# Optimization experiments

Hardware: AMD Instinct MI355X
Metric: run time of the kernel (lower is better)

## Reference

```python
import jax, jax.numpy as jnp
import numpy as np

N, E, D, H = 100000, 1000000, 64, 64  # nodes, edges, input_dim, output_dim
EPS = 1e-5


def _lin(k, fi, fo):
    return jax.random.normal(k, (fi, fo), jnp.float32) / np.sqrt(fi)


def setup_inputs() -> dict:
    key = jax.random.key(0)
    ks = jax.random.split(key, 8)
    x = jax.random.normal(ks[0], (N, D), jnp.float32)
    e = jax.random.uniform(ks[1], (E,), jnp.float32)
    edge_index = jax.random.randint(ks[2], (2, E), 0, N, dtype=jnp.int32)
    return {
        "x": x,
        "e": e,
        "edge_index": edge_index,
        "W1": _lin(ks[3], 2 * D, H), "b1": jnp.zeros((H,), jnp.float32),
        "g1": jnp.ones((H,), jnp.float32), "be1": jnp.zeros((H,), jnp.float32),
        "W2": _lin(ks[4], H, H), "b2": jnp.zeros((H,), jnp.float32),
        "g2": jnp.ones((H,), jnp.float32), "be2": jnp.zeros((H,), jnp.float32),
        "W3": _lin(ks[5], H, H), "b3": jnp.zeros((H,), jnp.float32),
    }


def _layer_norm(h, g, b):
    mu = jnp.mean(h, axis=-1, keepdims=True)
    var = jnp.mean(jnp.square(h - mu), axis=-1, keepdims=True)
    return (h - mu) * jax.lax.rsqrt(var + EPS) * g + b


def reference(x, e, edge_index, W1, b1, g1, be1, W2, b2, g2, be2, W3, b3):
    start, end = edge_index[0], edge_index[1]
    we = e[:, None]  # [E,1]
    # edge-weighted gather-multiply-scatter_add, both directions
    mi = jax.ops.segment_sum(we * x[start], end, num_segments=N) \
       + jax.ops.segment_sum(we * x[end], start, num_segments=N)  # [N,D]
    h = jnp.concatenate([mi, x], axis=1)  # [N,2D]
    h = jnp.tanh(_layer_norm(h @ W1 + b1, g1, be1))
    h = jnp.tanh(_layer_norm(h @ W2 + b2, g2, be2))
    return h @ W3 + b3  # [N,H]
```

## Files before the change

kernel.cpp:

```cpp
#include <hip/hip_runtime.h>

typedef unsigned int u32;
typedef int   v4i __attribute__((ext_vector_type(4)));
typedef float v4f __attribute__((ext_vector_type(4)));

#define NMAX 100000
#define EMAX 1000000
#define CAP 64
#define NSHMAX 12500

__device__ __align__(16) float g_mi[NMAX * 64];
__device__ int g_deg[8 * NSHMAX];
__device__ __align__(16) u32 g_adj[(size_t)8 * NSHMAX * CAP];

__global__ __launch_bounds__(256) void fill_sharded(
    const int* __restrict__ src, const int* __restrict__ dst,
    const float* __restrict__ ew, int E, int NSH, int nchunk)
{
    int group = blockIdx.x & 7;
    int chunk = blockIdx.x >> 3;
    int stride = nchunk * 256 * 4;
    for (int e0 = (chunk * 256 + threadIdx.x) * 4; e0 < E; e0 += stride) {
        if (e0 + 3 < E) {
            v4i s4 = __builtin_nontemporal_load((const v4i*)&src[e0]);
            v4i t4 = __builtin_nontemporal_load((const v4i*)&dst[e0]);
            v4f w4 = __builtin_nontemporal_load((const v4f*)&ew[e0]);
            #pragma unroll
            for (int j = 0; j < 4; j++) {
                int s = s4[j], t = t4[j];
                float w = w4[j];
                int w15 = (int)(w * 32768.f + 0.5f);
                if (w15 > 32767) w15 = 32767;
                if ((s & 7) == group) {
                    int idx = group * NSH + (s >> 3);
                    int p = atomicAdd(&g_deg[idx], 1);
                    if (p < CAP) g_adj[(size_t)idx * CAP + p] = ((u32)t << 15) | (u32)w15;
                }
                if ((t & 7) == group) {
                    int idx = group * NSH + (t >> 3);
                    int q = atomicAdd(&g_deg[idx], 1);
                    if (q < CAP) g_adj[(size_t)idx * CAP + q] = ((u32)s << 15) | (u32)w15;
                }
            }
        } else {
            for (int e = e0; e < E; e++) {
                int s = src[e], t = dst[e];
                float w = ew[e];
                int w15 = (int)(w * 32768.f + 0.5f);
                if (w15 > 32767) w15 = 32767;
                if ((s & 7) == group) {
                    int idx = group * NSH + (s >> 3);
                    int p = atomicAdd(&g_deg[idx], 1);
                    if (p < CAP) g_adj[(size_t)idx * CAP + p] = ((u32)t << 15) | (u32)w15;
                }
                if ((t & 7) == group) {
                    int idx = group * NSH + (t >> 3);
                    int q = atomicAdd(&g_deg[idx], 1);
                    if (q < CAP) g_adj[(size_t)idx * CAP + q] = ((u32)s << 15) | (u32)w15;
                }
            }
        }
    }
}

__global__ __launch_bounds__(256) void gather(const float* __restrict__ x,
                                              int N, int NSH) {
    int wid = (blockIdx.x * 256 + threadIdx.x) >> 6;
    int lane = threadIdx.x & 63;
    if (wid >= N) return;
    int idx = (wid & 7) * NSH + (wid >> 3);
    int cnt = g_deg[idx];
    if (lane == 0) g_deg[idx] = 0;
    if (cnt > CAP) cnt = CAP;
    const u32* row = g_adj + (size_t)idx * CAP;
    float acc = 0.f;

    for (int b = 0; b < cnt; b += 64) {
        int m = cnt - b;
        if (m > 64) m = 64;
        u32 ent = (lane < m) ? row[b + lane] : 0u;
        int nbr = (int)(ent >> 15);
        float wv = (float)(ent & 0x7FFFu) * (1.f / 32768.f);

        int j = 0;
        for (; j + 8 <= m; j += 8) {
            int   nn[8];
            float ww[8];
            #pragma unroll
            for (int u = 0; u < 8; u++) { nn[u] = __shfl(nbr, j + u); ww[u] = __shfl(wv, j + u); }
            float vv[8];
            #pragma unroll
            for (int u = 0; u < 8; u++) vv[u] = x[(size_t)nn[u] * 64 + lane];
            #pragma unroll
            for (int u = 0; u < 8; u++) acc = fmaf(ww[u], vv[u], acc);
        }
        for (; j + 4 <= m; j += 4) {
            int n0 = __shfl(nbr, j + 0);
            int n1 = __shfl(nbr, j + 1);
            int n2 = __shfl(nbr, j + 2);
            int n3 = __shfl(nbr, j + 3);
            float w0 = __shfl(wv, j + 0);
            float w1 = __shfl(wv, j + 1);
            float w2 = __shfl(wv, j + 2);
            float w3 = __shfl(wv, j + 3);
            float v0 = x[(size_t)n0 * 64 + lane];
            float v1 = x[(size_t)n1 * 64 + lane];
            float v2 = x[(size_t)n2 * 64 + lane];
            float v3 = x[(size_t)n3 * 64 + lane];
            acc = fmaf(w0, v0, acc);
            acc = fmaf(w1, v1, acc);
            acc = fmaf(w2, v2, acc);
            acc = fmaf(w3, v3, acc);
        }
        for (; j < m; j++) {
            int nb = __shfl(nbr, j);
            float w = __shfl(wv, j);
            acc = fmaf(w, x[(size_t)nb * 64 + lane], acc);
        }
    }
    g_mi[(size_t)wid * 64 + lane] = acc;
}

#define HS 68
#define SWF(f) ((((f) >> 2) & 7) << 2)

#define GEMM_PASS(WP) do {                                              \
    _Pragma("unroll 2")                                                 \
    for (int k = 0; k < 64; k++) {                                      \
        float a = ht[k * HS + (lane ^ SWF(k))];                         \
        const float* wp = (WP) + k * 64 + c0;                           \
        _Pragma("unroll")                                               \
        for (int c = 0; c < 16; c++) acc[c] = fmaf(a, wp[c], acc[c]);   \
    } } while (0)

__global__ __launch_bounds__(256, 8) void mlp(
    const float* __restrict__ x,
    const float* __restrict__ W1, const float* __restrict__ B1,
    const float* __restrict__ G1, const float* __restrict__ E1,
    const float* __restrict__ W2, const float* __restrict__ B2,
    const float* __restrict__ G2, const float* __restrict__ E2,
    const float* __restrict__ W3, const float* __restrict__ B3,
    float* __restrict__ out, int N)
{
    __shared__ float ht[64 * HS];
    __shared__ float lnb[4 * 64];

    int tid  = threadIdx.x;
    int lane = tid & 63;
    int c0   = __builtin_amdgcn_readfirstlane(tid >> 6) * 16;
    int n0 = blockIdx.x * 64;
    int nodes = N - n0; if (nodes > 64) nodes = 64;

    if (tid < 64) {
        lnb[tid]       = G1[tid];
        lnb[64 + tid]  = E1[tid];
        lnb[128 + tid] = G2[tid];
        lnb[192 + tid] = E2[tid];
    }

    float acc[16];
    #pragma unroll
    for (int c = 0; c < 16; c++) acc[c] = B1[c0 + c];

    #pragma unroll
    for (int it = 0; it < 4; it++) {
        int idx = tid + it * 256;
        int nd = idx >> 4, f4 = (idx & 15) * 4;
        v4f v = {0.f, 0.f, 0.f, 0.f};
        if (nd < nodes) v = *(const v4f*)&g_mi[(size_t)(n0 + nd) * 64 + f4];
        ht[(f4 + 0) * HS + (nd ^ SWF(f4 + 0))] = v[0];
        ht[(f4 + 1) * HS + (nd ^ SWF(f4 + 1))] = v[1];
        ht[(f4 + 2) * HS + (nd ^ SWF(f4 + 2))] = v[2];
        ht[(f4 + 3) * HS + (nd ^ SWF(f4 + 3))] = v[3];
    }
    __syncthreads();
    GEMM_PASS(W1);
    __syncthreads();

    #pragma unroll
    for (int it = 0; it < 4; it++) {
        int idx = tid + it * 256;
        int nd = idx >> 4, f4 = (idx & 15) * 4;
        v4f v = {0.f, 0.f, 0.f, 0.f};
        if (nd < nodes) v = *(const v4f*)&x[(size_t)(n0 + nd) * 64 + f4];
        ht[(f4 + 0) * HS + (nd ^ SWF(f4 + 0))] = v[0];
        ht[(f4 + 1) * HS + (nd ^ SWF(f4 + 1))] = v[1];
        ht[(f4 + 2) * HS + (nd ^ SWF(f4 + 2))] = v[2];
        ht[(f4 + 3) * HS + (nd ^ SWF(f4 + 3))] = v[3];
    }
    __syncthreads();
    GEMM_PASS(W1 + 64 * 64);
    __syncthreads();

    #pragma unroll
    for (int c = 0; c < 16; c++)
        ht[(c0 + c) * HS + (lane ^ SWF(c0 + c))] = acc[c];
    __syncthreads();

    if (tid < 64) {
        float mu = 0.f;
        for (int j = 0; j < 64; j++) mu += ht[j * HS + (tid ^ SWF(j))];
        mu *= (1.f / 64.f);
        float var = 0.f;
        for (int j = 0; j < 64; j++) { float d = ht[j * HS + (tid ^ SWF(j))] - mu; var += d * d; }
        var *= (1.f / 64.f);
        float rs = rsqrtf(var + 1e-5f);
        for (int j = 0; j < 64; j++) {
            float v = (ht[j * HS + (tid ^ SWF(j))] - mu) * rs * lnb[j] + lnb[64 + j];
            float ex = __expf(2.f * v);
            ht[j * HS + (tid ^ SWF(j))] = 1.f - 2.f / (ex + 1.f);
        }
    }
    __syncthreads();

    #pragma unroll
    for (int c = 0; c < 16; c++) acc[c] = B2[c0 + c];
    GEMM_PASS(W2);
    __syncthreads();
    #pragma unroll
    for (int c = 0; c < 16; c++)
        ht[(c0 + c) * HS + (lane ^ SWF(c0 + c))] = acc[c];
    __syncthreads();

    if (tid < 64) {
        float mu = 0.f;
        for (int j = 0; j < 64; j++) mu += ht[j * HS + (tid ^ SWF(j))];
        mu *= (1.f / 64.f);
        float var = 0.f;
        for (int j = 0; j < 64; j++) { float d = ht[j * HS + (tid ^ SWF(j))] - mu; var += d * d; }
        var *= (1.f / 64.f);
        float rs = rsqrtf(var + 1e-5f);
        for (int j = 0; j < 64; j++) {
            float v = (ht[j * HS + (tid ^ SWF(j))] - mu) * rs * lnb[128 + j] + lnb[192 + j];
            float ex = __expf(2.f * v);
            ht[j * HS + (tid ^ SWF(j))] = 1.f - 2.f / (ex + 1.f);
        }
    }
    __syncthreads();

    #pragma unroll
    for (int c = 0; c < 16; c++) acc[c] = B3[c0 + c];
    GEMM_PASS(W3);
    __syncthreads();
    #pragma unroll
    for (int c = 0; c < 16; c++)
        ht[(c0 + c) * HS + (lane ^ SWF(c0 + c))] = acc[c];
    __syncthreads();

    #pragma unroll
    for (int it = 0; it < 4; it++) {
        int idx = tid + it * 256;
        int nd = idx >> 4, f4 = (idx & 15) * 4;
        if (nd < nodes) {
            v4f v = { ht[(f4 + 0) * HS + (nd ^ SWF(f4 + 0))],
                      ht[(f4 + 1) * HS + (nd ^ SWF(f4 + 1))],
                      ht[(f4 + 2) * HS + (nd ^ SWF(f4 + 2))],
                      ht[(f4 + 3) * HS + (nd ^ SWF(f4 + 3))] };
            *(v4f*)&out[(size_t)(n0 + nd) * 64 + f4] = v;
        }
    }
}

extern "C" void kernel_launch(void* const* d_in, const int* in_sizes, int n_in,
                              void* d_out, int out_size, void* d_ws, size_t ws_size,
                              hipStream_t stream) {
    const float* x  = (const float*)d_in[0];
    const float* e  = (const float*)d_in[1];
    const int* ei   = (const int*)d_in[2];
    const float* W1 = (const float*)d_in[3];
    const float* b1 = (const float*)d_in[4];
    const float* g1 = (const float*)d_in[5];
    const float* be1= (const float*)d_in[6];
    const float* W2 = (const float*)d_in[7];
    const float* b2 = (const float*)d_in[8];
    const float* g2 = (const float*)d_in[9];
    const float* be2= (const float*)d_in[10];
    const float* W3 = (const float*)d_in[11];
    const float* b3 = (const float*)d_in[12];

    int N = in_sizes[0] / 64;
    int E = in_sizes[1];
    int NSH = (N + 7) / 8;

    int nchunk = 256;
    fill_sharded<<<8 * nchunk, 256, 0, stream>>>(ei, ei + E, e, E, NSH, nchunk);

    gather<<<(N * 64 + 255) / 256, 256, 0, stream>>>(x, N, NSH);

    mlp<<<(N + 63) / 64, 256, 0, stream>>>(
        x, W1, b1, g1, be1, W2, b2, g2, be2, W3, b3, (float*)d_out, N);
}
```

Before: 333.2 us.

## Gather four nodes per wavefront with 16-lane groups and float4 loads

The gather kernel now assigns four nodes to each 64-lane wavefront, with 16 lanes per node, and each lane loads a float4 of the neighbour's feature row instead of a single float. The goal is more memory-level parallelism per wave, wider loads, and fewer wavefronts for low-degree nodes. Every group in a wave iterates up to the wave's maximum degree in steps of 16. Invalid slots read the node's own row with zero weight, which adds redundant loads when degrees differ.

```diff
diff --git a/kernel.cpp b/kernel.cpp
--- a/kernel.cpp
+++ b/kernel.cpp
@@ -63,62 +63,46 @@
     }
 }
 
-__global__ __launch_bounds__(256) void gather(const float* __restrict__ x,
-                                              int N, int NSH) {
-    int wid = (blockIdx.x * 256 + threadIdx.x) >> 6;
+__global__ __launch_bounds__(256) void gather4(const float* __restrict__ x,
+                                               int N, int NSH) {
+    int wid  = (blockIdx.x * 256 + threadIdx.x) >> 6;
     int lane = threadIdx.x & 63;
-    if (wid >= N) return;
-    int idx = (wid & 7) * NSH + (wid >> 3);
-    int cnt = g_deg[idx];
-    if (lane == 0) g_deg[idx] = 0;
+    int sub  = lane >> 4;
+    int q    = lane & 15;
+    int node = wid * 4 + sub;
+    if (wid * 4 >= N) return;
+    bool nvalid = node < N;
+    int nodec = nvalid ? node : N - 1;
+    int idx = (nodec & 7) * NSH + (nodec >> 3);
+    int cnt = nvalid ? g_deg[idx] : 0;
+    if (nvalid && q == 0) g_deg[idx] = 0;
     if (cnt > CAP) cnt = CAP;
     const u32* row = g_adj + (size_t)idx * CAP;
-    float acc = 0.f;
-
-    for (int b = 0; b < cnt; b += 64) {
-        int m = cnt - b;
-        if (m > 64) m = 64;
-        u32 ent = (lane < m) ? row[b + lane] : 0u;
-        int nbr = (int)(ent >> 15);
-        float wv = (float)(ent & 0x7FFFu) * (1.f / 32768.f);
-
-        int j = 0;
-        for (; j + 8 <= m; j += 8) {
-            int   nn[8];
-            float ww[8];
-            #pragma unroll
-            for (int u = 0; u < 8; u++) { nn[u] = __shfl(nbr, j + u); ww[u] = __shfl(wv, j + u); }
-            float vv[8];
-            #pragma unroll
-            for (int u = 0; u < 8; u++) vv[u] = x[(size_t)nn[u] * 64 + lane];
-            #pragma unroll
-            for (int u = 0; u < 8; u++) acc = fmaf(ww[u], vv[u], acc);
-        }
-        for (; j + 4 <= m; j += 4) {
-            int n0 = __shfl(nbr, j + 0);
-            int n1 = __shfl(nbr, j + 1);
-            int n2 = __shfl(nbr, j + 2);
-            int n3 = __shfl(nbr, j + 3);
-            float w0 = __shfl(wv, j + 0);
-            float w1 = __shfl(wv, j + 1);
-            float w2 = __shfl(wv, j + 2);
-            float w3 = __shfl(wv, j + 3);
-            float v0 = x[(size_t)n0 * 64 + lane];
-            float v1 = x[(size_t)n1 * 64 + lane];
-            float v2 = x[(size_t)n2 * 64 + lane];
-            float v3 = x[(size_t)n3 * 64 + lane];
-            acc = fmaf(w0, v0, acc);
-            acc = fmaf(w1, v1, acc);
-            acc = fmaf(w2, v2, acc);
-            acc = fmaf(w3, v3, acc);
-        }
-        for (; j < m; j++) {
-            int nb = __shfl(nbr, j);
-            float w = __shfl(wv, j);
-            acc = fmaf(w, x[(size_t)nb * 64 + lane], acc);
-        }
-    }
-    g_mi[(size_t)wid * 64 + lane] = acc;
+
+    int mc = cnt;
+    mc = max(mc, __shfl_xor(mc, 16));
+    mc = max(mc, __shfl_xor(mc, 32));
+
+    int sgbase = sub << 4;
+    v4f acc = {0.f, 0.f, 0.f, 0.f};
+
+    for (int j0 = 0; j0 < mc; j0 += 16) {
+        u32 ec = row[j0 + q];
+        #pragma unroll
+        for (int u = 0; u < 16; u++) {
+            int j = j0 + u;
+            u32 e = __shfl(ec, sgbase + u);
+            bool val = (j < cnt);
+            int nb   = val ? (int)(e >> 15) : nodec;
+            float w  = val ? (float)(e & 0x7FFFu) * (1.f / 32768.f) : 0.f;
+            v4f xv = *(const v4f*)&x[(size_t)nb * 64 + (q << 2)];
+            acc[0] = fmaf(w, xv[0], acc[0]);
+            acc[1] = fmaf(w, xv[1], acc[1]);
+            acc[2] = fmaf(w, xv[2], acc[2]);
+            acc[3] = fmaf(w, xv[3], acc[3]);
+        }
+    }
+    if (nvalid) *(v4f*)&g_mi[(size_t)node * 64 + (q << 2)] = acc;
 }
 
 #define HS 68
@@ -285,7 +269,7 @@
     int nchunk = 256;
     fill_sharded<<<8 * nchunk, 256, 0, stream>>>(ei, ei + E, e, E, NSH, nchunk);
 
-    gather<<<(N * 64 + 255) / 256, 256, 0, stream>>>(x, N, NSH);
+    gather4<<<(N + 15) / 16, 256, 0, stream>>>(x, N, NSH);
 
     mlp<<<(N + 63) / 64, 256, 0, stream>>>(
         x, W1, b1, g1, be1, W2, b2, g2, be2, W3, b3, (float*)d_out, N);
```

After: 333.2 us. About the same (+0.0%).
